# Performance work log

Hardware: AMD Instinct MI355X
Metric: run time of the kernel (lower is better)

## Reference

```python
import jax, jax.numpy as jnp
import numpy as np

N, T, D, P, NB = 32768, 128, 32, 16, 15


def setup_inputs() -> dict:
    key = jax.random.key(0)
    ks = jax.random.split(key, 8)
    S = jax.random.normal(ks[0], (N, T, 1), dtype=jnp.float32)
    L_dyn = jax.random.normal(ks[1], (N, T, D), dtype=jnp.float32)
    C_static = jax.random.normal(ks[2], (N, P), dtype=jnp.float32)
    Y = jax.random.randint(ks[3], (N, T, 1), 0, 2).astype(jnp.float32)
    mask = jnp.ones((N, T), dtype=jnp.float32)
    return {
        "S": S, "L_dyn": L_dyn, "C_static": C_static, "Y": Y, "mask": mask,
        "psi": jnp.array([0.5], jnp.float32),
        "gamma_A": jnp.array([0.1], jnp.float32),
        "w_gamma_dyn": 0.05 * jax.random.normal(ks[4], (D,), dtype=jnp.float32),
        "w_gamma_static": 0.05 * jax.random.normal(ks[5], (P,), dtype=jnp.float32),
        "log_sigma_Z": jnp.array([-0.5], jnp.float32),
        "beta_0": jnp.array([-4.0], jnp.float32),
        "beta_Z": jnp.array([0.3], jnp.float32),
        "beta_bins": jnp.zeros((NB,), jnp.float32),
        "w_beta_dyn": 0.1 * jax.random.normal(ks[6], (D,), dtype=jnp.float32),
        "w_beta_static": 0.1 * jax.random.normal(ks[7], (P,), dtype=jnp.float32),
        "beta_time": jnp.array([0.03], jnp.float32),
    }


def reference(S, L_dyn, C_static, Y, mask, psi, gamma_A, w_gamma_dyn,
              w_gamma_static, log_sigma_Z, beta_0, beta_Z, beta_bins,
              w_beta_dyn, w_beta_static, beta_time):
    n, t_len = S.shape[0], S.shape[1]
    nb = beta_bins.shape[0]
    edges = jnp.linspace(-2.5, 2.5, nb + 1).astype(S.dtype)
    # torch.bucketize(s, edges[1:-1]) (right=False) == searchsorted side='left'
    idx = jnp.clip(jnp.searchsorted(edges[1:-1], S[..., 0], side='left'), 0, nb - 1)
    bin_eff = beta_bins[idx][..., None]            # (N,T,1) == (A_bin * beta_bins).sum(-1)
    sigma_sq = jnp.exp(log_sigma_Z)[0] ** 2        # sigma_Z^2
    gd = L_dyn @ w_gamma_dyn[:, None]              # (N,T,1) gamma_dyn(L)
    bd = L_dyn @ w_beta_dyn[:, None]               # (N,T,1) beta_dyn(L)
    gs = (C_static @ w_gamma_static)[:, None]      # (N,1) gamma_static(C)
    bs = (C_static @ w_beta_static)[:, None]       # (N,1) beta_static(C)
    tt = jnp.arange(t_len, dtype=S.dtype) / 30.0   # beta_time * (t/30)

    xs = (
        jnp.swapaxes(S, 0, 1),        # (T,N,1)
        jnp.swapaxes(gd, 0, 1),
        jnp.swapaxes(bd, 0, 1),
        jnp.swapaxes(bin_eff, 0, 1),
        jnp.swapaxes(Y, 0, 1),
        mask.T[:, :, None],           # (T,N,1)
        tt,
    )
    psi_s, gA, bZ, b0, bT = psi[0], gamma_A[0], beta_Z[0], beta_0[0], beta_time[0]

    def step(carry, x):
        Z_mean, Z_var, ll = carry
        A_t, gd_t, bd_t, be_t, Y_t, m_t, t_s = x
        # latent transition prior
        Z_pred_mean = psi_s * Z_mean + gA * A_t + gd_t + gs
        Z_pred_var = psi_s ** 2 * Z_var + sigma_sq
        # outcome probability
        logit = b0 + bZ * Z_pred_mean + be_t + bd_t + bs + bT * t_s
        prob = jax.nn.sigmoid(jnp.clip(logit, -20.0, 20.0))
        # approximate Kalman (Laplace) update from Y
        grad = (Y_t - prob) * bZ * m_t
        hess = bZ ** 2 * prob * (1.0 - prob) * m_t + 1e-6
        Z_post_var = 1.0 / (1.0 / (Z_pred_var + 1e-8) + hess)
        Z_post_mean = Z_pred_mean + Z_post_var * grad
        ll_t = ((Y_t * jnp.log(prob + 1e-10)
                 + (1.0 - Y_t) * jnp.log(1.0 - prob + 1e-10)) * m_t).sum()
        return (Z_post_mean, Z_post_var, ll + ll_t), (Z_post_mean, Z_post_var)

    init = (jnp.zeros((n, 1), S.dtype), jnp.ones((n, 1), S.dtype),
            jnp.zeros((), S.dtype))
    (_, _, ll), (Zf, Zv) = jax.lax.scan(step, init, xs)
    return jnp.swapaxes(Zf, 0, 1), jnp.swapaxes(Zv, 0, 1), ll
```

## Files before the change

### kernel.cpp

```cpp
#include <hip/hip_runtime.h>

#define T_LEN 128
#define D_DYN 32
#define P_STAT 16
#define NB_BINS 15

__global__ __launch_bounds__(256) void k_dots(
    const float4* __restrict__ L4,
    const float*  __restrict__ wg,
    const float*  __restrict__ wb,
    float* __restrict__ gd,
    float* __restrict__ bd,
    float* __restrict__ ll_out,
    int total_rows)
{
    int tid = blockIdx.x * blockDim.x + threadIdx.x;
    if (tid == 0) ll_out[0] = 0.0f;

    const int lane = tid & 7;
    const float4 wg4 = reinterpret_cast<const float4*>(wg)[lane];
    const float4 wb4 = reinterpret_cast<const float4*>(wb)[lane];

    const int group   = tid >> 3;
    const int ngroups = (gridDim.x * blockDim.x) >> 3;

    for (int row = group; row < total_rows; row += ngroups) {
        float4 v = L4[(size_t)row * 8 + lane];
        float g = v.x * wg4.x + v.y * wg4.y + v.z * wg4.z + v.w * wg4.w;
        float b = v.x * wb4.x + v.y * wb4.y + v.z * wb4.z + v.w * wb4.w;
        #pragma unroll
        for (int off = 1; off < 8; off <<= 1) {
            g += __shfl_xor(g, off, 64);
            b += __shfl_xor(b, off, 64);
        }
        if (lane == 0) { gd[row] = g; bd[row] = b; }
    }
}

__global__ __launch_bounds__(64) void k_scan(
    const float4* __restrict__ S4,
    const float4* __restrict__ Y4,
    const float4* __restrict__ M4,
    const float4* __restrict__ C4,
    const float*  __restrict__ wgs,
    const float*  __restrict__ wbs,
    const float*  __restrict__ p_psi,
    const float*  __restrict__ p_gA,
    const float*  __restrict__ p_lsz,
    const float*  __restrict__ p_b0,
    const float*  __restrict__ p_bZ,
    const float*  __restrict__ p_bbins,
    const float*  __restrict__ p_bT,
    float* zf,
    float* zv,
    float* ll_out,
    int n_seq)
{
    __shared__ float sbins[NB_BINS];
    if (threadIdx.x < NB_BINS) sbins[threadIdx.x] = p_bbins[threadIdx.x];
    __syncthreads();

    const int n = blockIdx.x * blockDim.x + threadIdx.x;
    if (n >= n_seq) return;

    const float psi  = p_psi[0];
    const float gA   = p_gA[0];
    const float e    = expf(p_lsz[0]);
    const float sig2 = e * e;
    const float b0   = p_b0[0];
    const float bZ   = p_bZ[0];
    const float bT   = p_bT[0];
    const float psi2 = psi * psi;
    const float bZ2  = bZ * bZ;

    float gs = 0.0f, bs = 0.0f;
    #pragma unroll
    for (int i = 0; i < P_STAT / 4; ++i) {
        float4 c  = C4[n * (P_STAT / 4) + i];
        float4 wg = reinterpret_cast<const float4*>(wgs)[i];
        float4 wb = reinterpret_cast<const float4*>(wbs)[i];
        gs += c.x * wg.x + c.y * wg.y + c.z * wg.z + c.w * wg.w;
        bs += c.x * wb.x + c.y * wb.y + c.z * wb.z + c.w * wb.w;
    }

    float zm = 0.0f, zvv = 1.0f, ll = 0.0f;
    const int base4 = n * (T_LEN / 4);

    float4* zf4 = reinterpret_cast<float4*>(zf);
    float4* zv4 = reinterpret_cast<float4*>(zv);

    float4 s4 = S4[base4], y4 = Y4[base4], m4 = M4[base4];
    float4 g4 = zf4[base4], b4 = zv4[base4];

    for (int tc = 0; tc < T_LEN / 4; ++tc) {
        float4 s4n, y4n, m4n, g4n, b4n;
        if (tc + 1 < T_LEN / 4) {
            s4n = S4[base4 + tc + 1];
            y4n = Y4[base4 + tc + 1];
            m4n = M4[base4 + tc + 1];
            g4n = zf4[base4 + tc + 1];
            b4n = zv4[base4 + tc + 1];
        }

        float pm[4], pv[4];
        const float* sp = &s4.x;  const float* yp = &y4.x;
        const float* mp = &m4.x;  const float* gp = &g4.x;
        const float* bp = &b4.x;
        #pragma unroll
        for (int j = 0; j < 4; ++j) {
            const int t = tc * 4 + j;
            const float s   = sp[j];
            const float y   = yp[j];
            const float m   = mp[j];
            const float gdv = gp[j];
            const float bdv = bp[j];

            int cnt = (int)fmaxf(0.0f, fminf(14.0f, ceilf(fmaf(s, 3.0f, 7.5f)) - 1.0f));
            const float be = sbins[cnt];

            const float zpm   = psi * zm + gA * s + gdv + gs;
            const float zpv   = psi2 * zvv + sig2;
            float logit = b0 + bZ * zpm + be + bdv + bs + bT * ((float)t / 30.0f);
            logit = fminf(fmaxf(logit, -20.0f), 20.0f);
            const float prob  = 1.0f / (1.0f + expf(-logit));
            const float grad  = (y - prob) * bZ * m;
            const float hess  = bZ2 * prob * (1.0f - prob) * m + 1e-6f;
            const float pvv   = 1.0f / (1.0f / (zpv + 1e-8f) + hess);
            const float pmm   = zpm + pvv * grad;
            ll += (y * logf(prob + 1e-10f) + (1.0f - y) * logf(1.0f - prob + 1e-10f)) * m;
            zm = pmm; zvv = pvv;
            pm[j] = pmm; pv[j] = pvv;
        }
        zf4[base4 + tc] = make_float4(pm[0], pm[1], pm[2], pm[3]);
        zv4[base4 + tc] = make_float4(pv[0], pv[1], pv[2], pv[3]);

        s4 = s4n; y4 = y4n; m4 = m4n; g4 = g4n; b4 = b4n;
    }

    #pragma unroll
    for (int off = 1; off < 64; off <<= 1) ll += __shfl_xor(ll, off, 64);
    if ((threadIdx.x & 63) == 0) atomicAdd(ll_out, ll);
}

extern "C" void kernel_launch(void* const* d_in, const int* in_sizes, int n_in,
                              void* d_out, int out_size, void* d_ws, size_t ws_size,
                              hipStream_t stream) {
    const float* S     = (const float*)d_in[0];
    const float* L     = (const float*)d_in[1];
    const float* C     = (const float*)d_in[2];
    const float* Y     = (const float*)d_in[3];
    const float* M     = (const float*)d_in[4];
    const float* psi   = (const float*)d_in[5];
    const float* gA    = (const float*)d_in[6];
    const float* wgd   = (const float*)d_in[7];
    const float* wgs   = (const float*)d_in[8];
    const float* lsz   = (const float*)d_in[9];
    const float* b0    = (const float*)d_in[10];
    const float* bZ    = (const float*)d_in[11];
    const float* bbins = (const float*)d_in[12];
    const float* wbd   = (const float*)d_in[13];
    const float* wbs   = (const float*)d_in[14];
    const float* bT    = (const float*)d_in[15];

    const int NT    = in_sizes[0];
    const int n_seq = NT / T_LEN;

    float* zf = (float*)d_out;
    float* zv = zf + NT;
    float* ll = zf + 2 * (size_t)NT;

    k_dots<<<2048, 256, 0, stream>>>(
        reinterpret_cast<const float4*>(L), wgd, wbd, zf, zv, ll, NT);

    k_scan<<<n_seq / 64, 64, 0, stream>>>(
        reinterpret_cast<const float4*>(S),
        reinterpret_cast<const float4*>(Y),
        reinterpret_cast<const float4*>(M),
        reinterpret_cast<const float4*>(C),
        wgs, wbs, psi, gA, lsz, b0, bZ, bbins, bT,
        zf, zv, ll, n_seq);
}
```

Measured before the change: 181.6 us.

## Fuse L_dyn dot products into the scan kernel with four lanes per sequence

Measured after the change: 177.8 us. 2.1% less time.

```diff
diff --git a/kernel.cpp b/kernel.cpp
--- a/kernel.cpp
+++ b/kernel.cpp
@@ -1,49 +1,18 @@
 #include <hip/hip_runtime.h>
 
 #define T_LEN 128
-#define D_DYN 32
-#define P_STAT 16
 #define NB_BINS 15
 
-__global__ __launch_bounds__(256) void k_dots(
-    const float4* __restrict__ L4,
-    const float*  __restrict__ wg,
-    const float*  __restrict__ wb,
-    float* __restrict__ gd,
-    float* __restrict__ bd,
-    float* __restrict__ ll_out,
-    int total_rows)
-{
-    int tid = blockIdx.x * blockDim.x + threadIdx.x;
-    if (tid == 0) ll_out[0] = 0.0f;
-
-    const int lane = tid & 7;
-    const float4 wg4 = reinterpret_cast<const float4*>(wg)[lane];
-    const float4 wb4 = reinterpret_cast<const float4*>(wb)[lane];
-
-    const int group   = tid >> 3;
-    const int ngroups = (gridDim.x * blockDim.x) >> 3;
-
-    for (int row = group; row < total_rows; row += ngroups) {
-        float4 v = L4[(size_t)row * 8 + lane];
-        float g = v.x * wg4.x + v.y * wg4.y + v.z * wg4.z + v.w * wg4.w;
-        float b = v.x * wb4.x + v.y * wb4.y + v.z * wb4.z + v.w * wb4.w;
-        #pragma unroll
-        for (int off = 1; off < 8; off <<= 1) {
-            g += __shfl_xor(g, off, 64);
-            b += __shfl_xor(b, off, 64);
-        }
-        if (lane == 0) { gd[row] = g; bd[row] = b; }
-    }
-}
-
-__global__ __launch_bounds__(64) void k_scan(
+__global__ __launch_bounds__(256) void k_fused(
     const float4* __restrict__ S4,
     const float4* __restrict__ Y4,
     const float4* __restrict__ M4,
     const float4* __restrict__ C4,
-    const float*  __restrict__ wgs,
-    const float*  __restrict__ wbs,
+    const float4* __restrict__ L4,
+    const float4* __restrict__ wgd4,
+    const float4* __restrict__ wbd4,
+    const float4* __restrict__ wgs4,
+    const float4* __restrict__ wbs4,
     const float*  __restrict__ p_psi,
     const float*  __restrict__ p_gA,
     const float*  __restrict__ p_lsz,
@@ -51,17 +20,20 @@
     const float*  __restrict__ p_bZ,
     const float*  __restrict__ p_bbins,
     const float*  __restrict__ p_bT,
-    float* zf,
-    float* zv,
-    float* ll_out,
-    int n_seq)
+    float* __restrict__ zf,
+    float* __restrict__ zv,
+    float* __restrict__ ll_out)
 {
     __shared__ float sbins[NB_BINS];
     if (threadIdx.x < NB_BINS) sbins[threadIdx.x] = p_bbins[threadIdx.x];
     __syncthreads();
 
-    const int n = blockIdx.x * blockDim.x + threadIdx.x;
-    if (n >= n_seq) return;
+    const int gtid = blockIdx.x * blockDim.x + threadIdx.x;
+    const int n = gtid >> 2;
+    const int s = gtid & 3;
+
+    const float4 wga = wgd4[s * 2],     wgb = wgd4[s * 2 + 1];
+    const float4 wba = wbd4[s * 2],     wbb = wbd4[s * 2 + 1];
 
     const float psi  = p_psi[0];
     const float gA   = p_gA[0];
@@ -73,73 +45,85 @@
     const float psi2 = psi * psi;
     const float bZ2  = bZ * bZ;
 
-    float gs = 0.0f, bs = 0.0f;
-    #pragma unroll
-    for (int i = 0; i < P_STAT / 4; ++i) {
-        float4 c  = C4[n * (P_STAT / 4) + i];
-        float4 wg = reinterpret_cast<const float4*>(wgs)[i];
-        float4 wb = reinterpret_cast<const float4*>(wbs)[i];
-        gs += c.x * wg.x + c.y * wg.y + c.z * wg.z + c.w * wg.w;
-        bs += c.x * wb.x + c.y * wb.y + c.z * wb.z + c.w * wb.w;
+    float gs, bs;
+    {
+        const float4 c  = C4[n * 4 + s];
+        const float4 wg = wgs4[s];
+        const float4 wb = wbs4[s];
+        gs = c.x * wg.x + c.y * wg.y + c.z * wg.z + c.w * wg.w;
+        bs = c.x * wb.x + c.y * wb.y + c.z * wb.z + c.w * wb.w;
+        gs += __shfl_xor(gs, 1, 64); gs += __shfl_xor(gs, 2, 64);
+        bs += __shfl_xor(bs, 1, 64); bs += __shfl_xor(bs, 2, 64);
     }
 
+    const size_t lb  = (size_t)n * T_LEN * 8 + (size_t)s * 2;
+    const int    sbi = n * (T_LEN / 4);
+
+    float4 Lc0 = L4[lb + 0*8], Lc1 = L4[lb + 0*8 + 1];
+    float4 Lc2 = L4[lb + 1*8], Lc3 = L4[lb + 1*8 + 1];
+    float4 Lc4 = L4[lb + 2*8], Lc5 = L4[lb + 2*8 + 1];
+    float4 Lc6 = L4[lb + 3*8], Lc7 = L4[lb + 3*8 + 1];
+    float4 sc = S4[sbi], yc = Y4[sbi], mc = M4[sbi];
+
     float zm = 0.0f, zvv = 1.0f, ll = 0.0f;
-    const int base4 = n * (T_LEN / 4);
 
-    float4* zf4 = reinterpret_cast<float4*>(zf);
-    float4* zv4 = reinterpret_cast<float4*>(zv);
+#define STEP(J, LA, LB, SS, YY, MM, PMOUT, PVOUT) do {                        \
+        const float s_v = (SS), y_v = (YY), m_v = (MM);                       \
+        float g   = LA.x*wga.x + LA.y*wga.y + LA.z*wga.z + LA.w*wga.w         \
+                  + LB.x*wgb.x + LB.y*wgb.y + LB.z*wgb.z + LB.w*wgb.w;        \
+        float bdv = LA.x*wba.x + LA.y*wba.y + LA.z*wba.z + LA.w*wba.w         \
+                  + LB.x*wbb.x + LB.y*wbb.y + LB.z*wbb.z + LB.w*wbb.w;        \
+        g   += __shfl_xor(g,   1, 64); g   += __shfl_xor(g,   2, 64);         \
+        bdv += __shfl_xor(bdv, 1, 64); bdv += __shfl_xor(bdv, 2, 64);         \
+        int cnt = (int)fmaxf(0.0f, fminf(14.0f,                               \
+                      ceilf(fmaf(s_v, 3.0f, 7.5f)) - 1.0f));                  \
+        const float be    = sbins[cnt];                                       \
+        const float zpm   = psi * zm + gA * s_v + g + gs;                     \
+        const float zpv   = psi2 * zvv + sig2;                                \
+        float logit = b0 + bZ * zpm + be + bdv + bs                           \
+                    + bT * ((float)(4 * k + (J)) / 30.0f);                    \
+        logit = fminf(fmaxf(logit, -20.0f), 20.0f);                           \
+        const float prob  = 1.0f / (1.0f + expf(-logit));                     \
+        const float grad  = (y_v - prob) * bZ * m_v;                          \
+        const float hess  = bZ2 * prob * (1.0f - prob) * m_v + 1e-6f;         \
+        const float pvv   = 1.0f / (1.0f / (zpv + 1e-8f) + hess);             \
+        const float pmm   = zpm + pvv * grad;                                 \
+        ll += (y_v * logf(prob + 1e-10f)                                      \
+             + (1.0f - y_v) * logf(1.0f - prob + 1e-10f)) * m_v;              \
+        zm = pmm; zvv = pvv; PMOUT = pmm; PVOUT = pvv;                        \
+    } while (0)
 
-    float4 s4 = S4[base4], y4 = Y4[base4], m4 = M4[base4];
-    float4 g4 = zf4[base4], b4 = zv4[base4];
+    for (int k = 0; k < T_LEN / 4; ++k) {
+        const int kn = (k + 1 < T_LEN / 4) ? (k + 1) : k;
+        const size_t lbn = lb + (size_t)(4 * kn) * 8;
+        float4 Ln0 = L4[lbn + 0*8], Ln1 = L4[lbn + 0*8 + 1];
+        float4 Ln2 = L4[lbn + 1*8], Ln3 = L4[lbn + 1*8 + 1];
+        float4 Ln4 = L4[lbn + 2*8], Ln5 = L4[lbn + 2*8 + 1];
+        float4 Ln6 = L4[lbn + 3*8], Ln7 = L4[lbn + 3*8 + 1];
+        float4 snn = S4[sbi + kn], ynn = Y4[sbi + kn], mnn = M4[sbi + kn];
 
-    for (int tc = 0; tc < T_LEN / 4; ++tc) {
-        float4 s4n, y4n, m4n, g4n, b4n;
-        if (tc + 1 < T_LEN / 4) {
-            s4n = S4[base4 + tc + 1];
-            y4n = Y4[base4 + tc + 1];
-            m4n = M4[base4 + tc + 1];
-            g4n = zf4[base4 + tc + 1];
-            b4n = zv4[base4 + tc + 1];
-        }
+        float pm0, pm1, pm2, pm3, pv0, pv1, pv2, pv3;
+        STEP(0, Lc0, Lc1, sc.x, yc.x, mc.x, pm0, pv0);
+        STEP(1, Lc2, Lc3, sc.y, yc.y, mc.y, pm1, pv1);
+        STEP(2, Lc4, Lc5, sc.z, yc.z, mc.z, pm2, pv2);
+        STEP(3, Lc6, Lc7, sc.w, yc.w, mc.w, pm3, pv3);
 
-        float pm[4], pv[4];
-        const float* sp = &s4.x;  const float* yp = &y4.x;
-        const float* mp = &m4.x;  const float* gp = &g4.x;
-        const float* bp = &b4.x;
-        #pragma unroll
-        for (int j = 0; j < 4; ++j) {
-            const int t = tc * 4 + j;
-            const float s   = sp[j];
-            const float y   = yp[j];
-            const float m   = mp[j];
-            const float gdv = gp[j];
-            const float bdv = bp[j];
+        const float pmsel = (s == 0) ? pm0 : (s == 1) ? pm1 : (s == 2) ? pm2 : pm3;
+        const float pvsel = (s == 0) ? pv0 : (s == 1) ? pv1 : (s == 2) ? pv2 : pv3;
+        const size_t oidx = (size_t)n * T_LEN + 4 * k + s;
+        zf[oidx] = pmsel;
+        zv[oidx] = pvsel;
 
-            int cnt = (int)fmaxf(0.0f, fminf(14.0f, ceilf(fmaf(s, 3.0f, 7.5f)) - 1.0f));
-            const float be = sbins[cnt];
+        Lc0 = Ln0; Lc1 = Ln1; Lc2 = Ln2; Lc3 = Ln3;
+        Lc4 = Ln4; Lc5 = Ln5; Lc6 = Ln6; Lc7 = Ln7;
+        sc = snn; yc = ynn; mc = mnn;
+    }
+#undef STEP
 
-            const float zpm   = psi * zm + gA * s + gdv + gs;
-            const float zpv   = psi2 * zvv + sig2;
-            float logit = b0 + bZ * zpm + be + bdv + bs + bT * ((float)t / 30.0f);
-            logit = fminf(fmaxf(logit, -20.0f), 20.0f);
-            const float prob  = 1.0f / (1.0f + expf(-logit));
-            const float grad  = (y - prob) * bZ * m;
-            const float hess  = bZ2 * prob * (1.0f - prob) * m + 1e-6f;
-            const float pvv   = 1.0f / (1.0f / (zpv + 1e-8f) + hess);
-            const float pmm   = zpm + pvv * grad;
-            ll += (y * logf(prob + 1e-10f) + (1.0f - y) * logf(1.0f - prob + 1e-10f)) * m;
-            zm = pmm; zvv = pvv;
-            pm[j] = pmm; pv[j] = pvv;
-        }
-        zf4[base4 + tc] = make_float4(pm[0], pm[1], pm[2], pm[3]);
-        zv4[base4 + tc] = make_float4(pv[0], pv[1], pv[2], pv[3]);
-
-        s4 = s4n; y4 = y4n; m4 = m4n; g4 = g4n; b4 = b4n;
-    }
-
+    float lv = (s == 0) ? ll : 0.0f;
     #pragma unroll
-    for (int off = 1; off < 64; off <<= 1) ll += __shfl_xor(ll, off, 64);
-    if ((threadIdx.x & 63) == 0) atomicAdd(ll_out, ll);
+    for (int off = 1; off < 64; off <<= 1) lv += __shfl_xor(lv, off, 64);
+    if ((threadIdx.x & 63) == 0) atomicAdd(ll_out, lv);
 }
 
 extern "C" void kernel_launch(void* const* d_in, const int* in_sizes, int n_in,
@@ -169,14 +153,20 @@
     float* zv = zf + NT;
     float* ll = zf + 2 * (size_t)NT;
 
-    k_dots<<<2048, 256, 0, stream>>>(
-        reinterpret_cast<const float4*>(L), wgd, wbd, zf, zv, ll, NT);
+    hipMemsetAsync((void*)ll, 0, sizeof(float), stream);
 
-    k_scan<<<n_seq / 64, 64, 0, stream>>>(
+    const int threads = 256;
+    const int blocks  = (n_seq * 4) / threads;
+    k_fused<<<blocks, threads, 0, stream>>>(
         reinterpret_cast<const float4*>(S),
         reinterpret_cast<const float4*>(Y),
         reinterpret_cast<const float4*>(M),
         reinterpret_cast<const float4*>(C),
-        wgs, wbs, psi, gA, lsz, b0, bZ, bbins, bT,
-        zf, zv, ll, n_seq);
+        reinterpret_cast<const float4*>(L),
+        reinterpret_cast<const float4*>(wgd),
+        reinterpret_cast<const float4*>(wbd),
+        reinterpret_cast<const float4*>(wgs),
+        reinterpret_cast<const float4*>(wbs),
+        psi, gA, lsz, b0, bZ, bbins, bT,
+        zf, zv, ll);
 }
```
